# Kernel optimization log

Measured on AMD Instinct MI355X. Metric: run time of the kernel, lower is better.

## Reference

```python
import jax, jax.numpy as jnp
import numpy as np
from jax import lax

VOCAB, EMB, HID, SEQ, BATCH = 50000, 512, 256, 64, 128


def _lstm_dir(x, Wih, Whh, bih, bhh):
    # x: (L,B,E); Wih: (4H,E); Whh: (4H,H); torch gate order i,f,g,o
    B = x.shape[1]
    H = Whh.shape[1]
    xg = jnp.einsum('lbe,ge->lbg', x, Wih) + (bih + bhh)  # precompute input contribution

    def step(carry, g_in):
        h, c = carry
        g = g_in + h @ Whh.T
        i, f, gg, o = jnp.split(g, 4, axis=-1)
        c = jax.nn.sigmoid(f) * c + jax.nn.sigmoid(i) * jnp.tanh(gg)
        h = jax.nn.sigmoid(o) * jnp.tanh(c)
        return (h, c), h

    z = jnp.zeros((B, H), x.dtype)
    _, hs = lax.scan(step, (z, z), xg)
    return hs  # (L,B,H)


def _bilstm(x, Wih_f, Whh_f, bih_f, bhh_f, Wih_b, Whh_b, bih_b, bhh_b):
    hf = _lstm_dir(x, Wih_f, Whh_f, bih_f, bhh_f)
    hb = _lstm_dir(x[::-1], Wih_b, Whh_b, bih_b, bhh_b)[::-1]
    return jnp.concatenate([hf, hb], axis=-1)  # (L,B,2H)


def _forward(tokens1, tokens2, emb, Wih_f, Whh_f, bih_f, bhh_f, Wih_b, Whh_b, bih_b, bhh_b):
    L, B = tokens1.shape
    w = (Wih_f, Whh_f, bih_f, bhh_f, Wih_b, Whh_b, bih_b, bhh_b)
    # original applies self.lstm_1 to BOTH sentences (lstm_2 unused)
    o1 = _bilstm(emb[tokens1], *w)  # (L,B,D)
    o2 = _bilstm(emb[tokens2], *w)
    D = o1.shape[-1]
    mp1 = o1.max(axis=0)  # adaptive_max_pool1d over time -> (B,D)
    # torch .view on contiguous (L,B,D): raw reshape, replicated faithfully
    att = jnp.einsum('bd,bdl->bl', mp1, o2.reshape(B, D, L))
    att_sm = jax.nn.softmax(att, axis=1)  # per-row softmax over L
    new_pool = jnp.einsum('bl,bld->bd', att_sm, o2.reshape(B, L, D))
    # commonWords: d[i] = LAST index j in sen1 with sen1[j]==sen2[i], else -1
    s1, s2 = tokens1.T, tokens2.T  # (B,L)
    match = s2[:, :, None] == s1[:, None, :]  # (B,L2,L1)
    d = jnp.max(jnp.where(match, jnp.arange(L)[None, None, :], -1), axis=2)  # (B,L)
    mask = (d > 1) & (s2 > 0)  # note strict > 1 as in original
    pos = jnp.clip(d, 0, L - 1)
    o1b = jnp.transpose(o1, (1, 0, 2))  # (B,L,D)
    gath1 = jnp.take_along_axis(o1b, pos[:, :, None], axis=1)  # outputs_1[d[i], b]
    neg = jnp.finfo(o1.dtype).min
    has = jnp.any(mask, axis=1)[:, None]
    e1h = jnp.where(has, jnp.max(jnp.where(mask[:, :, None], gath1, neg), axis=1), 0.0)
    o2b = jnp.transpose(o2, (1, 0, 2))
    e2h = jnp.where(has, jnp.max(jnp.where(mask[:, :, None], o2b, neg), axis=1), 0.0)
    sim = jnp.exp(-jnp.sum(jnp.abs(mp1 - new_pool), axis=1))
    return sim, e1h, e2h


def setup_inputs() -> dict:
    key = jax.random.key(0)
    ks = jax.random.split(key, 8)
    H4 = 4 * HID

    def w(k, shape, fan):
        return (jax.random.normal(k, shape, jnp.float32) / np.float32(np.sqrt(fan))).astype(jnp.float32)

    return {
        'tokens1': jax.random.randint(ks[0], (SEQ, BATCH), 0, VOCAB),
        'tokens2': jax.random.randint(ks[1], (SEQ, BATCH), 0, VOCAB),
        'emb': jax.random.normal(ks[2], (VOCAB, EMB), jnp.float32) * 0.1,
        'Wih_f': w(ks[3], (H4, EMB), EMB),
        'Whh_f': w(ks[4], (H4, HID), HID),
        'bih_f': jnp.full((H4,), 0.01, jnp.float32),
        'bhh_f': jnp.full((H4,), 0.01, jnp.float32),
        'Wih_b': w(ks[5], (H4, EMB), EMB),
        'Whh_b': w(ks[6], (H4, HID), HID),
        'bih_b': jnp.full((H4,), 0.01, jnp.float32),
        'bhh_b': jnp.full((H4,), 0.01, jnp.float32),
    }


def reference(tokens1, tokens2, emb, Wih_f, Whh_f, bih_f, bhh_f, Wih_b, Whh_b, bih_b, bhh_b):
    return _forward(tokens1, tokens2, emb, Wih_f, Whh_f, bih_f, bhh_f, Wih_b, Whh_b, bih_b, bhh_b)
```

## Files before the change

### kernel.cpp

```cpp
#include <hip/hip_runtime.h>
#include <hip/hip_bf16.h>
#include <math.h>

#define L_SEQ 64
#define NB    128
#define EMBD  512
#define HID   256
#define G4    1024
#define NCOL  2048
#define DDIM  512
#define MS    (L_SEQ*NB)
#define MTOT  (2*MS)

typedef __bf16 bf16_t;
typedef bf16_t bf16x4 __attribute__((ext_vector_type(4)));
typedef bf16_t bf16x8 __attribute__((ext_vector_type(8)));
typedef float  floatx4 __attribute__((ext_vector_type(4)));
typedef float  floatx8 __attribute__((ext_vector_type(8)));

__device__ __forceinline__ bf16x8 cvt_bf16x8(floatx8 v) {
    bf16x8 r;
    r[0]=(bf16_t)v[0]; r[1]=(bf16_t)v[1]; r[2]=(bf16_t)v[2]; r[3]=(bf16_t)v[3];
    r[4]=(bf16_t)v[4]; r[5]=(bf16_t)v[5]; r[6]=(bf16_t)v[6]; r[7]=(bf16_t)v[7];
    return r;
}

__device__ __forceinline__ void gload_lds16(const bf16_t* g, bf16_t* l) {
    __builtin_amdgcn_global_load_lds(
        (const __attribute__((address_space(1))) unsigned int*)(g),
        (__attribute__((address_space(3))) unsigned int*)(l), 16, 0, 0);
}

__device__ __forceinline__ float fsigmoid(float x) {
    return __builtin_amdgcn_rcpf(1.0f + __expf(-x));
}
__device__ __forceinline__ float ftanh(float x) {
    return 1.0f - 2.0f * __builtin_amdgcn_rcpf(__expf(2.0f*x) + 1.0f);
}

#define LDS_BARRIER() asm volatile("s_waitcnt lgkmcnt(0)\n\ts_barrier" ::: "memory")

__global__ __launch_bounds__(256) void k_pack_a(const int* __restrict__ t1,
                                                const int* __restrict__ t2,
                                                const float* __restrict__ emb,
                                                bf16_t* __restrict__ A)
{
    int gid = blockIdx.x*256 + threadIdx.x;
    int row = gid >> 6;
    int k8  = (gid & 63) * 8;
    int tok = (row < MS) ? t1[row] : t2[row - MS];
    floatx8 v = *(const floatx8*)(emb + (size_t)tok*EMBD + k8);
    *(bf16x8*)(A + (size_t)row*EMBD + k8) = cvt_bf16x8(v);
}

__global__ __launch_bounds__(256) void k_pack_w(
    const float* __restrict__ wih_f, const float* __restrict__ wih_b,
    const float* __restrict__ whh_f, const float* __restrict__ whh_b,
    const float* __restrict__ bih_f, const float* __restrict__ bhh_f,
    const float* __restrict__ bih_b, const float* __restrict__ bhh_b,
    bf16_t* __restrict__ B, bf16_t* __restrict__ whhB,
    float* __restrict__ bias)
{
    int gid = blockIdx.x*256 + threadIdx.x;
    if (gid < 131072) {
        int n  = gid >> 6;
        int k8 = (gid & 63) * 8;
        const float* src = (n >= 1024) ? (wih_b + (size_t)(n-1024)*EMBD)
                                       : (wih_f + (size_t)n*EMBD);
        *(bf16x8*)(B + (size_t)n*EMBD + k8) = cvt_bf16x8(*(const floatx8*)(src + k8));
    } else if (gid < 196608) {
        int g2 = gid - 131072;
        int r2 = g2 >> 5;
        int k8 = (g2 & 31) * 8;
        const float* src = (r2 >= 1024) ? (whh_b + (size_t)(r2-1024)*HID)
                                        : (whh_f + (size_t)r2*HID);
        *(bf16x8*)(whhB + (size_t)r2*HID + k8) = cvt_bf16x8(*(const floatx8*)(src + k8));
    } else {
        int n = gid - 196608;
        bias[n] = (n >= 1024) ? (bih_b[n-1024] + bhh_b[n-1024])
                              : (bih_f[n] + bhh_f[n]);
    }
}

__global__ __launch_bounds__(256) void xg_gemm4(const bf16_t* __restrict__ A,
                                                const bf16_t* __restrict__ B,
                                                const float* __restrict__ bias,
                                                bf16_t* __restrict__ xgT)
{
    __shared__ bf16_t As[128*32];
    __shared__ bf16_t Bs[128*32];
    const int tid  = threadIdx.x;
    const int wid  = tid >> 6;
    const int lane = tid & 63;
    const int l15  = lane & 15;
    const int quad = lane >> 4;

    const int bid  = blockIdx.y * 16 + blockIdx.x;
    const int virt = (bid & 7) * 256 + (bid >> 3);
    const int bx   = virt & 15;
    const int by   = virt >> 4;
    const int m0   = by * 128;
    const int n0   = bx * 128;
    const int mw   = (wid & 1) * 64;
    const int nw   = (wid >> 1) * 64;

    float biasv[4];
#pragma unroll
    for (int ni = 0; ni < 4; ++ni) biasv[ni] = bias[n0 + nw + ni*16 + l15];

    const int srow = tid >> 2;
    const int sk8  = (tid & 3) * 8;

    floatx4 acc[4][4] = {};
    for (int kk = 0; kk < EMBD; kk += 32) {
#pragma unroll
        for (int inst = 0; inst < 2; ++inst) {
            gload_lds16(A + (size_t)(m0 + inst*64 + srow)*EMBD + kk + sk8,
                        As + inst*2048 + wid*512);
            gload_lds16(B + (size_t)(n0 + inst*64 + srow)*EMBD + kk + sk8,
                        Bs + inst*2048 + wid*512);
        }
        __syncthreads();
        bf16x8 a[4], b[4];
#pragma unroll
        for (int mi = 0; mi < 4; ++mi)
            a[mi] = *(const bf16x8*)(As + (mw + mi*16 + l15)*32 + quad*8);
#pragma unroll
        for (int ni = 0; ni < 4; ++ni)
            b[ni] = *(const bf16x8*)(Bs + (nw + ni*16 + l15)*32 + quad*8);
#pragma unroll
        for (int mi = 0; mi < 4; ++mi)
#pragma unroll
            for (int ni = 0; ni < 4; ++ni)
                acc[mi][ni] = __builtin_amdgcn_mfma_f32_16x16x32_bf16(
                                  a[mi], b[ni], acc[mi][ni], 0, 0, 0);
        __syncthreads();
    }

    const int sent = by >> 6;
    const int l    = by & 63;
    const int dir  = n0 >> 10;
    const int s2   = sent*2 + dir;
#pragma unroll
    for (int mi = 0; mi < 4; ++mi)
#pragma unroll
        for (int ni = 0; ni < 4; ++ni) {
            int gcol = (n0 & 1023) + nw + ni*16 + l15;
            int b    = mw + mi*16 + quad*4;
            int ch   = b >> 4;
            int bi   = b & 15;
            bf16x4 v;
#pragma unroll
            for (int r = 0; r < 4; ++r) v[r] = (bf16_t)(acc[mi][ni][r] + biasv[ni]);
            *(bf16x4*)(xgT + ((size_t)((s2*8 + ch)*64 + l)*1024 + gcol)*16 + bi) = v;
        }
}

__global__
__attribute__((amdgpu_flat_work_group_size(1024, 1024), amdgpu_waves_per_eu(4, 4)))
void lstm_scan8(
    const bf16_t* __restrict__ whhB,
    const bf16_t* __restrict__ xgT,
    float* __restrict__ o1, float* __restrict__ o2)
{
    extern __shared__ char smem[];
    bf16_t* hb = (bf16_t*)smem;
    bf16_t* BL = (bf16_t*)(smem + 16384);

    const int tid  = threadIdx.x;
    const int wv   = tid >> 6;
    const int lane = tid & 63;
    const int l15  = lane & 15;
    const int quad = lane >> 4;
    const int s2   = blockIdx.y;
    const int sent = s2 >> 1;
    const int dr   = s2 & 1;
    const int chunk= blockIdx.x;
    const int b0   = chunk * 16;
    float* o = sent ? o2 : o1;
    const bf16_t* bb = whhB + (size_t)dr * (1024*HID);


#pragma unroll
    for (int g = 0; g < 4; ++g) {
        const int col = g*256 + wv*16 + l15;
#pragma unroll
        for (int ksl = 0; ksl < 2; ++ksl)
            gload_lds16(bb + (size_t)col*HID + (4+ksl)*32 + quad*8,
                        BL + (size_t)((wv*4 + g)*2 + ksl)*512);
    }

    bf16x8 bwc[4][4];
#pragma unroll
    for (int g = 0; g < 4; ++g) {
        const bf16_t* cp = bb + (size_t)(g*256 + wv*16 + l15)*HID + quad*8;
#pragma unroll
        for (int ks = 0; ks < 4; ++ks)
            bwc[g][ks] = *(const volatile bf16x8*)(cp + ks*32);
    }

    for (int i = tid; i < 4096; i += 1024) hb[i] = (bf16_t)0.0f;
    __syncthreads();

    float cst[4] = {};
    int pp = 0;

    for (int t = 0; t < L_SEQ; ++t) {
        const int lt = dr ? (L_SEQ-1-t) : t;
        asm volatile("" ::: "memory");

        bf16x4 xvc[4];
        {
            const bf16_t* xp = xgT + (size_t)((s2*8 + chunk)*64 + lt)*16384;
#pragma unroll
            for (int g = 0; g < 4; ++g)
                xvc[g] = *(const bf16x4*)(xp + (size_t)(g*256 + wv*16 + l15)*16
                                          + quad*4);
        }

        floatx4 acc[4] = {};
        if (t > 0) {
            bf16x8 sb[4];
#pragma unroll
            for (int g = 0; g < 4; ++g) {
                const bf16_t* cp = bb + (size_t)(g*256 + wv*16 + l15)*HID;
                sb[g] = *(const bf16x8*)(cp + 6*32 + quad*8);
            }

            const bf16_t* fr = hb + pp*4096;
#pragma unroll
            for (int ks = 0; ks < 4; ++ks) {
                bf16x8 af = *(const bf16x8*)(fr + ((ks*4 + quad)*16 + l15)*8);
#pragma unroll
                for (int g = 0; g < 4; ++g)
                    acc[g] = __builtin_amdgcn_mfma_f32_16x16x32_bf16(
                                 af, bwc[g][ks], acc[g], 0, 0, 0);
            }
            {
                bf16x8 af6 = *(const bf16x8*)(fr + ((6*4 + quad)*16 + l15)*8);
#pragma unroll
                for (int g = 0; g < 4; ++g)
                    acc[g] = __builtin_amdgcn_mfma_f32_16x16x32_bf16(
                                 af6, sb[g], acc[g], 0, 0, 0);
            }
#pragma unroll
            for (int g = 0; g < 4; ++g) {
                const bf16_t* cp = bb + (size_t)(g*256 + wv*16 + l15)*HID;
                sb[g] = *(const bf16x8*)(cp + 7*32 + quad*8);
            }
#pragma unroll
            for (int ksl = 0; ksl < 2; ++ksl) {
                bf16x8 af = *(const bf16x8*)(fr + (((4+ksl)*4 + quad)*16 + l15)*8);
#pragma unroll
                for (int g = 0; g < 4; ++g) {
                    bf16x8 bl = *(const bf16x8*)(BL + (size_t)((wv*4 + g)*2 + ksl)*512
                                                 + lane*8);
                    acc[g] = __builtin_amdgcn_mfma_f32_16x16x32_bf16(
                                 af, bl, acc[g], 0, 0, 0);
                }
            }
            {
                bf16x8 af7 = *(const bf16x8*)(fr + ((7*4 + quad)*16 + l15)*8);
#pragma unroll
                for (int g = 0; g < 4; ++g)
                    acc[g] = __builtin_amdgcn_mfma_f32_16x16x32_bf16(
                                 af7, sb[g], acc[g], 0, 0, 0);
            }
        }

        bf16_t* fw = hb + (pp^1)*4096;
        const int j = wv*16 + l15;
        float* orow = o + (size_t)(lt*NB + b0)*DDIM + dr*HID + j;
#pragma unroll
        for (int r = 0; r < 4; ++r) {
            const int m = quad*4 + r;
            float gi = acc[0][r] + (float)xvc[0][r];
            float gf = acc[1][r] + (float)xvc[1][r];
            float gg = acc[2][r] + (float)xvc[2][r];
            float go = acc[3][r] + (float)xvc[3][r];
            float cv = fsigmoid(gf)*cst[r] + fsigmoid(gi)*ftanh(gg);
            cst[r] = cv;
            float hv = fsigmoid(go)*ftanh(cv);
            orow[(size_t)m*DDIM] = hv;
            fw[((j >> 3)*16 + m)*8 + (j & 7)] = (bf16_t)hv;
        }
        LDS_BARRIER();
        pp ^= 1;
    }
}

__global__ __launch_bounds__(256) void k_att(const float* __restrict__ o1,
                                             const float* __restrict__ o2,
                                             float* __restrict__ sim)
{
    const int b   = blockIdx.x;
    const int tid = threadIdx.x;
    const int l   = tid & 63;
    const int cp  = tid >> 6;
    __shared__ float smp[512];
    __shared__ float spart[256];
    __shared__ float satt[64], sexp[64], ssm[64];
    __shared__ float red[256];

    const float* o2b = o2 + (size_t)b*32768;

#pragma unroll
    for (int h = 0; h < 2; ++h) {
        const int d = tid + h*256;
        float m = -3.402823466e+38f;
        for (int ll = 0; ll < 64; ++ll)
            m = fmaxf(m, o1[(size_t)ll*(NB*DDIM) + b*DDIM + d]);
        smp[d] = m;
    }
    __syncthreads();

    float p = 0.0f;
    for (int d = cp*128; d < cp*128 + 128; ++d)
        p += smp[d] * o2b[d*64 + l];
    spart[tid] = p;
    __syncthreads();
    if (tid < 64)
        satt[tid] = spart[tid] + spart[tid+64] + spart[tid+128] + spart[tid+192];
    __syncthreads();
    if (tid < 64) {
        float mx = satt[0];
        for (int i = 1; i < 64; ++i) mx = fmaxf(mx, satt[i]);
        sexp[tid] = expf(satt[tid] - mx);
    }
    __syncthreads();
    if (tid < 64) {
        float s = 0.0f;
        for (int i = 0; i < 64; ++i) s += sexp[i];
        ssm[tid] = sexp[tid] / s;
    }
    __syncthreads();

    float np0 = 0.0f, np1 = 0.0f;
    for (int l2 = 0; l2 < 64; ++l2) {
        float smv = ssm[l2];
        np0 += smv * o2b[l2*DDIM + tid];
        np1 += smv * o2b[l2*DDIM + tid + 256];
    }
    float diff = fabsf(smp[tid] - np0) + fabsf(smp[tid+256] - np1);
    red[tid] = diff;
    __syncthreads();
    for (int s = 128; s > 0; s >>= 1) {
        if (tid < s) red[tid] += red[tid + s];
        __syncthreads();
    }
    if (tid == 0) sim[b] = expf(-red[0]);
}

__global__ __launch_bounds__(256) void k_common(
    const int*   __restrict__ t1, const int* __restrict__ t2,
    const float* __restrict__ o1, const float* __restrict__ o2,
    float* __restrict__ e1h, float* __restrict__ e2h)
{
    const int b   = blockIdx.x;
    const int tid = threadIdx.x;
    __shared__ int ss1[64];
    __shared__ int smask[64];
    __shared__ int spos[64];
    __shared__ int sany;
    if (tid == 0) sany = 0;
    if (tid < 64) ss1[tid] = t1[tid*NB + b];
    __syncthreads();
    if (tid < 64) {
        int s2 = t2[tid*NB + b];
        int dmax = -1;
        for (int j = 0; j < 64; ++j)
            if (ss1[j] == s2) dmax = j;
        int mk = (dmax > 1) && (s2 > 0);
        smask[tid] = mk;
        spos[tid]  = dmax < 0 ? 0 : dmax;
        if (mk) sany = 1;
    }
    __syncthreads();
    int has = sany;
#pragma unroll
    for (int half = 0; half < 2; ++half) {
        int dd = tid + half*256;
        float m1 = -3.402823466e+38f, m2 = -3.402823466e+38f;
        for (int i = 0; i < 64; ++i) {
            if (smask[i]) {
                m1 = fmaxf(m1, o1[(size_t)spos[i]*(NB*DDIM) + b*DDIM + dd]);
                m2 = fmaxf(m2, o2[(size_t)i      *(NB*DDIM) + b*DDIM + dd]);
            }
        }
        e1h[b*DDIM + dd] = has ? m1 : 0.0f;
        e2h[b*DDIM + dd] = has ? m2 : 0.0f;
    }
}

extern "C" void kernel_launch(void* const* d_in, const int* in_sizes, int n_in,
                              void* d_out, int out_size, void* d_ws, size_t ws_size,
                              hipStream_t stream)
{
    (void)in_sizes; (void)n_in; (void)out_size; (void)ws_size;
    const int*   t1    = (const int*)d_in[0];
    const int*   t2    = (const int*)d_in[1];
    const float* emb   = (const float*)d_in[2];
    const float* wih_f = (const float*)d_in[3];
    const float* whh_f = (const float*)d_in[4];
    const float* bih_f = (const float*)d_in[5];
    const float* bhh_f = (const float*)d_in[6];
    const float* wih_b = (const float*)d_in[7];
    const float* whh_b = (const float*)d_in[8];
    const float* bih_b = (const float*)d_in[9];
    const float* bhh_b = (const float*)d_in[10];
    float* out = (float*)d_out;

    char* ws = (char*)d_ws;
    size_t off = 0;
    auto carve = [&](size_t bytes) -> void* {
        void* p = ws + off;
        off = (off + bytes + 255) & ~(size_t)255;
        return p;
    };
    float*  o1    = (float*)carve(sizeof(float)*(size_t)L_SEQ*NB*DDIM);
    float*  o2    = (float*)carve(sizeof(float)*(size_t)L_SEQ*NB*DDIM);
    bf16_t* whhB  = (bf16_t*)carve(sizeof(bf16_t)*2*1024*HID);
    bf16_t* Bw    = (bf16_t*)carve(sizeof(bf16_t)*(size_t)NCOL*EMBD);
    float*  bias  = (float*)carve(sizeof(float)*NCOL);
    bf16_t* xgT   = (bf16_t*)carve(sizeof(bf16_t)*(size_t)MTOT*NCOL);
    bf16_t* A     = (bf16_t*)o1;

    hipFuncSetAttribute((const void*)lstm_scan8,
                        hipFuncAttributeMaxDynamicSharedMemorySize, 147456);

    hipLaunchKernelGGL(k_pack_a, dim3(4096), dim3(256), 0, stream, t1, t2, emb, A);
    hipLaunchKernelGGL(k_pack_w, dim3(776),  dim3(256), 0, stream,
                       wih_f, wih_b, whh_f, whh_b,
                       bih_f, bhh_f, bih_b, bhh_b, Bw, whhB, bias);

    hipLaunchKernelGGL(xg_gemm4, dim3(16, 128), dim3(256), 0, stream, A, Bw, bias, xgT);

    hipLaunchKernelGGL(lstm_scan8, dim3(8, 4), dim3(1024), 147456, stream,
                       whhB, xgT, o1, o2);

    hipLaunchKernelGGL(k_att,    dim3(128), dim3(256), 0, stream, o1, o2, out);
    hipLaunchKernelGGL(k_common, dim3(128), dim3(256), 0, stream,
                       t1, t2, o1, o2, out + NB, out + NB + NB*DDIM);
}
```

Baseline: 619.1 us.

## Fuse embedding gather into input-projection GEMM with LDS-resident A tile

Removes the separate embedding pack kernel and fuses the token gather plus fp32-to-bf16 conversion into the xg GEMM. Each 512-thread block gathers 64 token rows into a swizzled 64KB LDS tile, then loops over all 2048 output columns in four passes, streaming weight tiles through LDS. This avoids writing and re-reading the bf16 A matrix in global memory and drops one launch. In exchange the grid shrinks to 256 large blocks with one barrier-bound weight-load loop per pass, which may reduce occupancy and latency hiding.

```diff
diff --git a/kernel.cpp b/kernel.cpp
--- a/kernel.cpp
+++ b/kernel.cpp
@@ -39,19 +39,6 @@
 }
 
 #define LDS_BARRIER() asm volatile("s_waitcnt lgkmcnt(0)\n\ts_barrier" ::: "memory")
-
-__global__ __launch_bounds__(256) void k_pack_a(const int* __restrict__ t1,
-                                                const int* __restrict__ t2,
-                                                const float* __restrict__ emb,
-                                                bf16_t* __restrict__ A)
-{
-    int gid = blockIdx.x*256 + threadIdx.x;
-    int row = gid >> 6;
-    int k8  = (gid & 63) * 8;
-    int tok = (row < MS) ? t1[row] : t2[row - MS];
-    floatx8 v = *(const floatx8*)(emb + (size_t)tok*EMBD + k8);
-    *(bf16x8*)(A + (size_t)row*EMBD + k8) = cvt_bf16x8(v);
-}
 
 __global__ __launch_bounds__(256) void k_pack_w(
     const float* __restrict__ wih_f, const float* __restrict__ wih_b,
@@ -82,78 +69,97 @@
     }
 }
 
-__global__ __launch_bounds__(256) void xg_gemm4(const bf16_t* __restrict__ A,
-                                                const bf16_t* __restrict__ B,
-                                                const float* __restrict__ bias,
-                                                bf16_t* __restrict__ xgT)
-{
-    __shared__ bf16_t As[128*32];
-    __shared__ bf16_t Bs[128*32];
+__global__
+__attribute__((amdgpu_flat_work_group_size(512, 512)))
+void k_embgemm(const int* __restrict__ t1, const int* __restrict__ t2,
+               const float* __restrict__ emb,
+               const bf16_t* __restrict__ Bw, const float* __restrict__ bias,
+               bf16_t* __restrict__ xgT)
+{
+    extern __shared__ char smem[];
+    bf16_t* Al = (bf16_t*)smem;
+    bf16_t* Bs = (bf16_t*)(smem + 65536);
+
     const int tid  = threadIdx.x;
-    const int wid  = tid >> 6;
+    const int wv   = tid >> 6;
     const int lane = tid & 63;
     const int l15  = lane & 15;
     const int quad = lane >> 4;
-
-    const int bid  = blockIdx.y * 16 + blockIdx.x;
-    const int virt = (bid & 7) * 256 + (bid >> 3);
-    const int bx   = virt & 15;
-    const int by   = virt >> 4;
-    const int m0   = by * 128;
-    const int n0   = bx * 128;
-    const int mw   = (wid & 1) * 64;
-    const int nw   = (wid >> 1) * 64;
-
-    float biasv[4];
-#pragma unroll
-    for (int ni = 0; ni < 4; ++ni) biasv[ni] = bias[n0 + nw + ni*16 + l15];
-
-    const int srow = tid >> 2;
-    const int sk8  = (tid & 3) * 8;
-
-    floatx4 acc[4][4] = {};
-    for (int kk = 0; kk < EMBD; kk += 32) {
-#pragma unroll
-        for (int inst = 0; inst < 2; ++inst) {
-            gload_lds16(A + (size_t)(m0 + inst*64 + srow)*EMBD + kk + sk8,
-                        As + inst*2048 + wid*512);
-            gload_lds16(B + (size_t)(n0 + inst*64 + srow)*EMBD + kk + sk8,
-                        Bs + inst*2048 + wid*512);
-        }
-        __syncthreads();
-        bf16x8 a[4], b[4];
+    const int blk  = blockIdx.x;
+    const int m0   = blk * 64;
+
+    {
+        const int rw   = tid >> 3;
+        const int c0   = tid & 7;
+        const int grow = m0 + rw;
+        const int tok  = (grow < MS) ? t1[grow] : t2[grow - MS];
+        const float* er = emb + (size_t)tok*EMBD;
+#pragma unroll
+        for (int i = 0; i < 8; ++i) {
+            const int c  = c0 + i*8;
+            floatx8 v = *(const floatx8*)(er + c*8);
+            const int cs = c ^ (rw & 7);
+            *(bf16x8*)(Al + rw*512 + cs*8) = cvt_bf16x8(v);
+        }
+    }
+    __syncthreads();
+
+    const int sent = m0 >> 13;
+    const int l    = (m0 >> 7) & 63;
+    const int chb  = (blk & 1) * 4;
+
+    for (int p = 0; p < 4; ++p) {
+        float biasv[4];
+#pragma unroll
+        for (int ni = 0; ni < 4; ++ni)
+            biasv[ni] = bias[p*512 + wv*64 + ni*16 + l15];
+
+        floatx4 acc[4][4] = {};
+        for (int kk = 0; kk < 16; ++kk) {
+#pragma unroll
+            for (int it = 0; it < 4; ++it) {
+                const int idx = it*512 + tid;
+                const int col = idx >> 2;
+                const int k8  = (idx & 3) * 8;
+                gload_lds16(Bw + (size_t)(p*512 + col)*EMBD + kk*32 + k8,
+                            Bs + (size_t)(it*512 + wv*64)*8);
+            }
+            __syncthreads();
+
+            bf16x8 a[4], b[4];
+#pragma unroll
+            for (int mi = 0; mi < 4; ++mi) {
+                const int arow = mi*16 + l15;
+                a[mi] = *(const bf16x8*)(Al + arow*512
+                                         + (((kk*4 + quad) ^ (arow & 7))*8));
+            }
+#pragma unroll
+            for (int ni = 0; ni < 4; ++ni)
+                b[ni] = *(const bf16x8*)(Bs + (wv*64 + ni*16 + l15)*32 + quad*8);
+#pragma unroll
+            for (int mi = 0; mi < 4; ++mi)
+#pragma unroll
+                for (int ni = 0; ni < 4; ++ni)
+                    acc[mi][ni] = __builtin_amdgcn_mfma_f32_16x16x32_bf16(
+                                      a[mi], b[ni], acc[mi][ni], 0, 0, 0);
+            __syncthreads();
+        }
+
+        const int s2 = sent*2 + (p >> 1);
 #pragma unroll
         for (int mi = 0; mi < 4; ++mi)
-            a[mi] = *(const bf16x8*)(As + (mw + mi*16 + l15)*32 + quad*8);
-#pragma unroll
-        for (int ni = 0; ni < 4; ++ni)
-            b[ni] = *(const bf16x8*)(Bs + (nw + ni*16 + l15)*32 + quad*8);
-#pragma unroll
-        for (int mi = 0; mi < 4; ++mi)
-#pragma unroll
-            for (int ni = 0; ni < 4; ++ni)
-                acc[mi][ni] = __builtin_amdgcn_mfma_f32_16x16x32_bf16(
-                                  a[mi], b[ni], acc[mi][ni], 0, 0, 0);
-        __syncthreads();
-    }
-
-    const int sent = by >> 6;
-    const int l    = by & 63;
-    const int dir  = n0 >> 10;
-    const int s2   = sent*2 + dir;
-#pragma unroll
-    for (int mi = 0; mi < 4; ++mi)
-#pragma unroll
-        for (int ni = 0; ni < 4; ++ni) {
-            int gcol = (n0 & 1023) + nw + ni*16 + l15;
-            int b    = mw + mi*16 + quad*4;
-            int ch   = b >> 4;
-            int bi   = b & 15;
-            bf16x4 v;
-#pragma unroll
-            for (int r = 0; r < 4; ++r) v[r] = (bf16_t)(acc[mi][ni][r] + biasv[ni]);
-            *(bf16x4*)(xgT + ((size_t)((s2*8 + ch)*64 + l)*1024 + gcol)*16 + bi) = v;
-        }
+#pragma unroll
+            for (int ni = 0; ni < 4; ++ni) {
+                const int gcol = (p & 1)*512 + wv*64 + ni*16 + l15;
+                const int ch   = chb + mi;
+                bf16x4 v;
+#pragma unroll
+                for (int r = 0; r < 4; ++r)
+                    v[r] = (bf16_t)(acc[mi][ni][r] + biasv[ni]);
+                *(bf16x4*)(xgT + ((size_t)((s2*8 + ch)*64 + l)*1024 + gcol)*16
+                           + quad*4) = v;
+            }
+    }
 }
 
 __global__
@@ -179,7 +185,6 @@
     const int b0   = chunk * 16;
     float* o = sent ? o2 : o1;
     const bf16_t* bb = whhB + (size_t)dr * (1024*HID);
-
 
 #pragma unroll
     for (int g = 0; g < 4; ++g) {
@@ -423,17 +428,18 @@
     bf16_t* Bw    = (bf16_t*)carve(sizeof(bf16_t)*(size_t)NCOL*EMBD);
     float*  bias  = (float*)carve(sizeof(float)*NCOL);
     bf16_t* xgT   = (bf16_t*)carve(sizeof(bf16_t)*(size_t)MTOT*NCOL);
-    bf16_t* A     = (bf16_t*)o1;
 
     hipFuncSetAttribute((const void*)lstm_scan8,
                         hipFuncAttributeMaxDynamicSharedMemorySize, 147456);
-
-    hipLaunchKernelGGL(k_pack_a, dim3(4096), dim3(256), 0, stream, t1, t2, emb, A);
-    hipLaunchKernelGGL(k_pack_w, dim3(776),  dim3(256), 0, stream,
+    hipFuncSetAttribute((const void*)k_embgemm,
+                        hipFuncAttributeMaxDynamicSharedMemorySize, 98304);
+
+    hipLaunchKernelGGL(k_pack_w, dim3(776), dim3(256), 0, stream,
                        wih_f, wih_b, whh_f, whh_b,
                        bih_f, bhh_f, bih_b, bhh_b, Bw, whhB, bias);
 
-    hipLaunchKernelGGL(xg_gemm4, dim3(16, 128), dim3(256), 0, stream, A, Bw, bias, xgT);
+    hipLaunchKernelGGL(k_embgemm, dim3(256), dim3(512), 98304, stream,
+                       t1, t2, emb, Bw, bias, xgT);
 
     hipLaunchKernelGGL(lstm_scan8, dim3(8, 4), dim3(1024), 147456, stream,
                        whhB, xgT, o1, o2);
```

After: 646.1 us. 1.04x slower.

## Prefetch next-step input gates in LSTM scan and drop GEMM block swizzle

Applied to the files above, without the earlier changes.

The LSTM recurrence now loads the precomputed input-gate values for step t+1 during step t, after folding the current values into the accumulators. This takes that global load off the critical path at the start of each serial step. Separately, the xg GEMM drops its block-index swizzle in favour of a plain grid mapping, which may change L2 locality. The prefetch keeps a few more values live in registers across the loop.

```diff
diff --git a/kernel.cpp b/kernel.cpp
--- a/kernel.cpp
+++ b/kernel.cpp
@@ -94,13 +94,8 @@
     const int lane = tid & 63;
     const int l15  = lane & 15;
     const int quad = lane >> 4;
-
-    const int bid  = blockIdx.y * 16 + blockIdx.x;
-    const int virt = (bid & 7) * 256 + (bid >> 3);
-    const int bx   = virt & 15;
-    const int by   = virt >> 4;
-    const int m0   = by * 128;
-    const int n0   = bx * 128;
+    const int m0   = blockIdx.y * 128;
+    const int n0   = blockIdx.x * 128;
     const int mw   = (wid & 1) * 64;
     const int nw   = (wid >> 1) * 64;
 
@@ -137,8 +132,8 @@
         __syncthreads();
     }
 
-    const int sent = by >> 6;
-    const int l    = by & 63;
+    const int sent = blockIdx.y >> 6;
+    const int l    = blockIdx.y & 63;
     const int dir  = n0 >> 10;
     const int s2   = sent*2 + dir;
 #pragma unroll
@@ -158,7 +153,7 @@
 
 __global__
 __attribute__((amdgpu_flat_work_group_size(1024, 1024), amdgpu_waves_per_eu(4, 4)))
-void lstm_scan8(
+void lstm_scan10(
     const bf16_t* __restrict__ whhB,
     const bf16_t* __restrict__ xgT,
     float* __restrict__ o1, float* __restrict__ o2)
@@ -179,6 +174,7 @@
     const int b0   = chunk * 16;
     float* o = sent ? o2 : o1;
     const bf16_t* bb = whhB + (size_t)dr * (1024*HID);
+    const bf16_t* xbase = xgT + (size_t)((s2*8 + chunk)*64)*16384;
 
 
 #pragma unroll
@@ -205,18 +201,19 @@
     float cst[4] = {};
     int pp = 0;
 
+    bf16x4 xvc[4];
+    {
+        const int lt0 = dr ? (L_SEQ-1) : 0;
+        const bf16_t* xp = xbase + (size_t)lt0*16384;
+#pragma unroll
+        for (int g = 0; g < 4; ++g)
+            xvc[g] = *(const bf16x4*)(xp + (size_t)(g*256 + wv*16 + l15)*16
+                                      + quad*4);
+    }
+
     for (int t = 0; t < L_SEQ; ++t) {
         const int lt = dr ? (L_SEQ-1-t) : t;
         asm volatile("" ::: "memory");
-
-        bf16x4 xvc[4];
-        {
-            const bf16_t* xp = xgT + (size_t)((s2*8 + chunk)*64 + lt)*16384;
-#pragma unroll
-            for (int g = 0; g < 4; ++g)
-                xvc[g] = *(const bf16x4*)(xp + (size_t)(g*256 + wv*16 + l15)*16
-                                          + quad*4);
-        }
 
         floatx4 acc[4] = {};
         if (t > 0) {
@@ -268,19 +265,31 @@
             }
         }
 
+#pragma unroll
+        for (int g = 0; g < 4; ++g)
+#pragma unroll
+            for (int r = 0; r < 4; ++r)
+                acc[g][r] += (float)xvc[g][r];
+
+        {
+            const int tn  = (t < L_SEQ-1) ? t+1 : t;
+            const int ltn = dr ? (L_SEQ-1-tn) : tn;
+            const bf16_t* xp = xbase + (size_t)ltn*16384;
+#pragma unroll
+            for (int g = 0; g < 4; ++g)
+                xvc[g] = *(const bf16x4*)(xp + (size_t)(g*256 + wv*16 + l15)*16
+                                          + quad*4);
+        }
+
         bf16_t* fw = hb + (pp^1)*4096;
         const int j = wv*16 + l15;
         float* orow = o + (size_t)(lt*NB + b0)*DDIM + dr*HID + j;
 #pragma unroll
         for (int r = 0; r < 4; ++r) {
             const int m = quad*4 + r;
-            float gi = acc[0][r] + (float)xvc[0][r];
-            float gf = acc[1][r] + (float)xvc[1][r];
-            float gg = acc[2][r] + (float)xvc[2][r];
-            float go = acc[3][r] + (float)xvc[3][r];
-            float cv = fsigmoid(gf)*cst[r] + fsigmoid(gi)*ftanh(gg);
+            float cv = fsigmoid(acc[1][r])*cst[r] + fsigmoid(acc[0][r])*ftanh(acc[2][r]);
             cst[r] = cv;
-            float hv = fsigmoid(go)*ftanh(cv);
+            float hv = fsigmoid(acc[3][r])*ftanh(cv);
             orow[(size_t)m*DDIM] = hv;
             fw[((j >> 3)*16 + m)*8 + (j & 7)] = (bf16_t)hv;
         }
@@ -425,7 +434,7 @@
     bf16_t* xgT   = (bf16_t*)carve(sizeof(bf16_t)*(size_t)MTOT*NCOL);
     bf16_t* A     = (bf16_t*)o1;
 
-    hipFuncSetAttribute((const void*)lstm_scan8,
+    hipFuncSetAttribute((const void*)lstm_scan10,
                         hipFuncAttributeMaxDynamicSharedMemorySize, 147456);
 
     hipLaunchKernelGGL(k_pack_a, dim3(4096), dim3(256), 0, stream, t1, t2, emb, A);
@@ -435,7 +444,7 @@
 
     hipLaunchKernelGGL(xg_gemm4, dim3(16, 128), dim3(256), 0, stream, A, Bw, bias, xgT);
 
-    hipLaunchKernelGGL(lstm_scan8, dim3(8, 4), dim3(1024), 147456, stream,
+    hipLaunchKernelGGL(lstm_scan10, dim3(8, 4), dim3(1024), 147456, stream,
                        whhB, xgT, o1, o2);
 
     hipLaunchKernelGGL(k_att,    dim3(128), dim3(256), 0, stream, o1, o2, out);
```

Result: no change. 614.5 us (-0.7%).
